# Optimization experiments

Measured on AMD Instinct MI355X. Metric: run time of the kernel, lower is better.

## Reference

```python
import jax, jax.numpy as jnp
import numpy as np
import math

B, S, D, H = 2, 2048, 2048, 16
DH = D // H  # 128

def setup_inputs() -> dict:
    key = jax.random.key(0)
    ks = jax.random.split(key, 5)
    x = jax.random.normal(ks[0], (B, S, D), dtype=jnp.float32)
    # causal mask: 1 where attendable, 0 where masked (masked_fill at mask==0)
    mask = jnp.tril(jnp.ones((S, S), dtype=jnp.int32))[None, None, :, :]
    wq = jax.random.normal(ks[1], (D, D), dtype=jnp.float32) * (1.0 / math.sqrt(D))
    wk = jax.random.normal(ks[2], (D, D), dtype=jnp.float32) * (1.0 / math.sqrt(D))
    wv = jax.random.normal(ks[3], (D, D), dtype=jnp.float32) * (1.0 / math.sqrt(D))
    wo = jax.random.normal(ks[4], (D, D), dtype=jnp.float32) * (1.0 / math.sqrt(D))
    return {"x": x, "mask": mask, "wq": wq, "wk": wk, "wv": wv, "wo": wo}

def reference(x, mask, wq, wk, wv, wo):
    b, s, d = x.shape
    # nn.Linear(d,d,bias=False): y = x @ W.T
    q = (x @ wq.T).reshape(b, s, H, DH).transpose(0, 2, 1, 3)  # [b,h,s,dh]
    k = (x @ wk.T).reshape(b, s, H, DH).transpose(0, 2, 1, 3)
    v = (x @ wv.T).reshape(b, s, H, DH).transpose(0, 2, 1, 3)
    scores = jnp.einsum('bhqd,bhkd->bhqk', q, k) / math.sqrt(DH)
    scores = jnp.where(mask == 0, jnp.float32(-1e9), scores)
    attn_weights = jax.nn.softmax(scores, axis=-1)
    attn_out = jnp.einsum('bhqk,bhkd->bhqd', attn_weights, v)
    attn_out = attn_out.transpose(0, 2, 1, 3).reshape(b, s, d)
    output = attn_out @ wo.T
    return (output, attn_weights)
```

## Files before the change

kernel.cpp:

```cpp
#include <hip/hip_runtime.h>
#include <hip/hip_bf16.h>
#include <cstdint>
#include <cstddef>

#define BATCH 2
#define S_LEN 2048
#define D_DIM 2048
#define NH 16
#define DHEAD 128
#define NXE ((size_t)BATCH * S_LEN * D_DIM)
#define NWE ((size_t)D_DIM * D_DIM)

typedef __bf16 bf16;
typedef __attribute__((ext_vector_type(8))) __bf16 bf16x8;
typedef __attribute__((ext_vector_type(4))) __bf16 bf16x4;
typedef __attribute__((ext_vector_type(4))) float f32x4;

__device__ __forceinline__ void async16(const void* g, void* l) {
  __builtin_amdgcn_global_load_lds((__attribute__((address_space(1))) void*)g,
                                   (__attribute__((address_space(3))) void*)l,
                                   16, 0, 0);
}

__global__ __launch_bounds__(256) void cast_kernel(const float4* __restrict__ in,
                                                   bf16x4* __restrict__ out, int n4) {
  int i = blockIdx.x * 256 + threadIdx.x;
  if (i < n4) {
    float4 v = in[i];
    bf16x4 o;
    o[0] = (bf16)v.x; o[1] = (bf16)v.y; o[2] = (bf16)v.z; o[3] = (bf16)v.w;
    out[i] = o;
  }
}

__global__ __launch_bounds__(256) void gemm_qkv(const bf16* __restrict__ A,
                                                const bf16* __restrict__ Wf,
                                                bf16* __restrict__ C0) {
  __shared__ __align__(16) bf16 As[128 * 32];
  __shared__ __align__(16) bf16 Bs[128 * 32];
  const int tid = threadIdx.x;
  const int wave = tid >> 6, lane = tid & 63;
  const int quad = lane >> 4, l16 = lane & 15;
  const int wm = (wave >> 1) * 64, wn = (wave & 1) * 64;
  const int m0 = blockIdx.y * 128, n0 = blockIdx.x * 128;
  const int K = D_DIM;

  f32x4 acc[4][4];
#pragma unroll
  for (int i = 0; i < 4; ++i)
#pragma unroll
    for (int j = 0; j < 4; ++j) acc[i][j] = (f32x4){0.f, 0.f, 0.f, 0.f};

  for (int k0 = 0; k0 < K; k0 += 32) {
    __syncthreads();
#pragma unroll
    for (int i = 0; i < 2; ++i) {
      int c = i * 256 + tid;
      int row = c & 127, k8 = c >> 7;
      async16(A + (size_t)(m0 + row) * K + k0 + k8 * 8, (void*)(As + (i * 256 + wave * 64) * 8));
      async16(Wf + (size_t)(n0 + row) * K + k0 + k8 * 8, (void*)(Bs + (i * 256 + wave * 64) * 8));
    }
    __builtin_amdgcn_s_waitcnt(0);
    __syncthreads();
    bf16x8 af[4], bfr[4];
#pragma unroll
    for (int i = 0; i < 4; ++i)
      af[i] = *(const bf16x8*)(As + (quad * 128 + wm + i * 16 + l16) * 8);
#pragma unroll
    for (int j = 0; j < 4; ++j)
      bfr[j] = *(const bf16x8*)(Bs + (quad * 128 + wn + j * 16 + l16) * 8);
#pragma unroll
    for (int i = 0; i < 4; ++i)
#pragma unroll
      for (int j = 0; j < 4; ++j)
        acc[i][j] = __builtin_amdgcn_mfma_f32_16x16x32_bf16(af[i], bfr[j], acc[i][j], 0, 0, 0);
  }
  const int mat = n0 >> 11;
  const int cb = n0 & 2047;
  bf16* Cm = C0 + (size_t)mat * NXE;
#pragma unroll
  for (int i = 0; i < 4; ++i)
#pragma unroll
    for (int j = 0; j < 4; ++j)
#pragma unroll
      for (int r = 0; r < 4; ++r) {
        int row = m0 + wm + i * 16 + quad * 4 + r;
        int col = cb + wn + j * 16 + l16;
        Cm[(size_t)row * D_DIM + col] = (bf16)acc[i][j][r];
      }
}

__global__ __launch_bounds__(256) void gemm_out(const bf16* __restrict__ A,
                                                const bf16* __restrict__ Bm,
                                                float* __restrict__ Cf) {
  __shared__ __align__(16) bf16 As[128 * 32];
  __shared__ __align__(16) bf16 Bs[128 * 32];
  const int tid = threadIdx.x;
  const int wave = tid >> 6, lane = tid & 63;
  const int quad = lane >> 4, l16 = lane & 15;
  const int wm = (wave >> 1) * 64, wn = (wave & 1) * 64;
  const int m0 = blockIdx.y * 128, n0 = blockIdx.x * 128;
  const int K = D_DIM, N = D_DIM;

  f32x4 acc[4][4];
#pragma unroll
  for (int i = 0; i < 4; ++i)
#pragma unroll
    for (int j = 0; j < 4; ++j) acc[i][j] = (f32x4){0.f, 0.f, 0.f, 0.f};

  for (int k0 = 0; k0 < K; k0 += 32) {
    __syncthreads();
#pragma unroll
    for (int i = 0; i < 2; ++i) {
      int c = i * 256 + tid;
      int row = c & 127, k8 = c >> 7;
      async16(A + (size_t)(m0 + row) * K + k0 + k8 * 8, (void*)(As + (i * 256 + wave * 64) * 8));
      async16(Bm + (size_t)(n0 + row) * K + k0 + k8 * 8, (void*)(Bs + (i * 256 + wave * 64) * 8));
    }
    __builtin_amdgcn_s_waitcnt(0);
    __syncthreads();
    bf16x8 af[4], bfr[4];
#pragma unroll
    for (int i = 0; i < 4; ++i)
      af[i] = *(const bf16x8*)(As + (quad * 128 + wm + i * 16 + l16) * 8);
#pragma unroll
    for (int j = 0; j < 4; ++j)
      bfr[j] = *(const bf16x8*)(Bs + (quad * 128 + wn + j * 16 + l16) * 8);
#pragma unroll
    for (int i = 0; i < 4; ++i)
#pragma unroll
      for (int j = 0; j < 4; ++j)
        acc[i][j] = __builtin_amdgcn_mfma_f32_16x16x32_bf16(af[i], bfr[j], acc[i][j], 0, 0, 0);
  }
#pragma unroll
  for (int i = 0; i < 4; ++i)
#pragma unroll
    for (int j = 0; j < 4; ++j)
#pragma unroll
      for (int r = 0; r < 4; ++r) {
        int row = m0 + wm + i * 16 + quad * 4 + r;
        int col = n0 + wn + j * 16 + l16;
        Cf[(size_t)row * N + col] = acc[i][j][r];
      }
}

__global__ __launch_bounds__(256) void transpose_v(const bf16* __restrict__ V,
                                                   bf16* __restrict__ Vt) {
  __shared__ __align__(16) bf16 tileT[64 * 80];
  const int tid = threadIdx.x;
  const int bh = blockIdx.z, b = bh >> 4, h = bh & 15;
  const int s0 = blockIdx.x * 64, d0 = blockIdx.y * 64;
  const int i = tid >> 3;
  const int jc = (tid & 7) * 8;
#pragma unroll
  for (int ii = 0; ii < 2; ++ii) {
    int si = i + ii * 32;
    bf16x8 v = *(const bf16x8*)(V + (size_t)(b * S_LEN + s0 + si) * D_DIM + h * DHEAD + d0 + jc);
#pragma unroll
    for (int u = 0; u < 8; ++u) tileT[(jc + u) * 80 + si] = v[u];
  }
  __syncthreads();
#pragma unroll
  for (int jj = 0; jj < 2; ++jj) {
    int jr = i + jj * 32;
    bf16x8 o = *(const bf16x8*)(tileT + jr * 80 + jc);
    *(bf16x8*)(Vt + ((size_t)bh * DHEAD + d0 + jr) * S_LEN + s0 + jc) = o;
  }
}

__global__ __launch_bounds__(256, 3) void attn_kernel(const bf16* __restrict__ Q,
                                                      const bf16* __restrict__ Kg,
                                                      const bf16* __restrict__ Vt,
                                                      float* __restrict__ P,
                                                      bf16* __restrict__ AO) {
  __shared__ __align__(16) bf16 KVs[128 * 128];
  __shared__ __align__(16) bf16 Ps[4][16 * 128];
  const int tid = threadIdx.x, wave = tid >> 6, lane = tid & 63;
  const int quad = lane >> 4, l16 = lane & 15;
  const int bh = blockIdx.y, b = bh >> 4, h = bh & 15;
  const int mt = (int)gridDim.x - 1 - (int)blockIdx.x;
  const int m0 = mt * 64;
  const int ntc = mt / 2 + 1;
  const bf16* Qh = Q + (size_t)b * S_LEN * D_DIM + h * DHEAD;
  const bf16* Kh = Kg + (size_t)b * S_LEN * D_DIM + h * DHEAD;
  const bf16* Vth = Vt + (size_t)bh * DHEAD * S_LEN;
  float* Pb = P + ((size_t)bh * S_LEN + m0) * S_LEN;
  const float scale = 0.08838834764831845f;

  bf16x8 aq[4];
  const bf16* qrow = Qh + (size_t)(m0 + wave * 16 + l16) * D_DIM + quad * 8;
#pragma unroll
  for (int kt = 0; kt < 4; ++kt) aq[kt] = *(const bf16x8*)(qrow + kt * 32);

  const int row_base = m0 + wave * 16 + quad * 4;
  float mrun[4], lrun[4];
#pragma unroll
  for (int r = 0; r < 4; ++r) { mrun[r] = -1e30f; lrun[r] = 0.f; }

  for (int t = 0; t < ntc; ++t) {
    const int n0 = t * 128;
    __syncthreads();
#pragma unroll
    for (int i = 0; i < 8; ++i) {
      int c = i * 256 + tid;
      int row = c & 127, k8 = c >> 7;
      async16(Kh + (size_t)(n0 + row) * D_DIM + k8 * 8, (void*)(KVs + (i * 256 + wave * 64) * 8));
    }
    __builtin_amdgcn_s_waitcnt(0);
    __syncthreads();
    f32x4 sacc[8];
#pragma unroll
    for (int jt = 0; jt < 8; ++jt) sacc[jt] = (f32x4){0.f, 0.f, 0.f, 0.f};
#pragma unroll
    for (int jt = 0; jt < 8; ++jt)
#pragma unroll
      for (int kt = 0; kt < 4; ++kt) {
        bf16x8 bk = *(const bf16x8*)(KVs + ((kt * 4 + quad) * 128 + jt * 16 + l16) * 8);
        sacc[jt] = __builtin_amdgcn_mfma_f32_16x16x32_bf16(aq[kt], bk, sacc[jt], 0, 0, 0);
      }
    const bool full = (n0 + 127 <= m0);
#pragma unroll
    for (int r = 0; r < 4; ++r) {
      const int rowg = row_base + r;
      float s[8], tmax = -3.0e38f;
#pragma unroll
      for (int jt = 0; jt < 8; ++jt) {
        float v = sacc[jt][r] * scale;
        if (!full) { int colg = n0 + jt * 16 + l16; v = (colg <= rowg) ? v : -3.0e38f; }
        s[jt] = v;
        tmax = fmaxf(tmax, v);
      }
      float mnew = fmaxf(mrun[r], tmax);
      float ps = 0.f;
#pragma unroll
      for (int jt = 0; jt < 8; ++jt) ps += __expf(s[jt] - mnew);
      lrun[r] = lrun[r] * __expf(mrun[r] - mnew) + ps;
      mrun[r] = mnew;
    }
  }
  float linv[4];
#pragma unroll
  for (int r = 0; r < 4; ++r) {
    float m = mrun[r], l = lrun[r];
#pragma unroll
    for (int off = 1; off < 16; off <<= 1) {
      float mo = __shfl_xor(m, off);
      float lo = __shfl_xor(l, off);
      float mn = fmaxf(m, mo);
      l = l * __expf(m - mn) + lo * __expf(mo - mn);
      m = mn;
    }
    mrun[r] = m;
    linv[r] = 1.0f / l;
  }

  f32x4 oacc[8];
#pragma unroll
  for (int jt = 0; jt < 8; ++jt) oacc[jt] = (f32x4){0.f, 0.f, 0.f, 0.f};
  bf16* myPs = Ps[wave];

  for (int t = 0; t < 16; ++t) {
    const int n0 = t * 128;
    if (t < ntc) {
      __syncthreads();
#pragma unroll
      for (int i = 0; i < 8; ++i) {
        int c = i * 256 + tid;
        int row = c & 127, k8 = c >> 7;
        async16(Kh + (size_t)(n0 + row) * D_DIM + k8 * 8, (void*)(KVs + (i * 256 + wave * 64) * 8));
      }
      __builtin_amdgcn_s_waitcnt(0);
      __syncthreads();
      f32x4 sacc[8];
#pragma unroll
      for (int jt = 0; jt < 8; ++jt) sacc[jt] = (f32x4){0.f, 0.f, 0.f, 0.f};
#pragma unroll
      for (int jt = 0; jt < 8; ++jt)
#pragma unroll
        for (int kt = 0; kt < 4; ++kt) {
          bf16x8 bk = *(const bf16x8*)(KVs + ((kt * 4 + quad) * 128 + jt * 16 + l16) * 8);
          sacc[jt] = __builtin_amdgcn_mfma_f32_16x16x32_bf16(aq[kt], bk, sacc[jt], 0, 0, 0);
        }
      const bool full = (n0 + 127 <= m0);
#pragma unroll
      for (int jt = 0; jt < 8; ++jt)
#pragma unroll
        for (int r = 0; r < 4; ++r) {
          float e = __expf(sacc[jt][r] * scale - mrun[r]) * linv[r];
          if (!full) {
            int colg = n0 + jt * 16 + l16;
            e = (colg <= row_base + r) ? e : 0.f;
          }
          int kk = jt * 16 + l16, m = quad * 4 + r;
          myPs[((kk >> 3) * 16 + m) * 8 + (kk & 7)] = (bf16)e;
        }
      asm volatile("s_waitcnt lgkmcnt(0)" ::: "memory");
      bf16x8 ap[4];
#pragma unroll
      for (int kt = 0; kt < 4; ++kt)
        ap[kt] = *(const bf16x8*)(myPs + ((kt * 4 + quad) * 16 + l16) * 8);
#pragma unroll
      for (int i = 0; i < 8; ++i) {
        int idx = i * 64 + lane;
        int row = idx >> 5, c0 = (idx & 31) * 4;
        bf16x4 pv = *(const bf16x4*)(myPs + ((c0 >> 3) * 16 + row) * 8 + (c0 & 7));
        float4 o = make_float4((float)pv[0], (float)pv[1], (float)pv[2], (float)pv[3]);
        *(float4*)(Pb + (size_t)(wave * 16 + row) * S_LEN + n0 + c0) = o;
      }
      __syncthreads();
#pragma unroll
      for (int i = 0; i < 8; ++i) {
        int c = i * 256 + tid;
        int row = c & 127, k8 = c >> 7;
        async16(Vth + (size_t)row * S_LEN + n0 + k8 * 8, (void*)(KVs + (i * 256 + wave * 64) * 8));
      }
      __builtin_amdgcn_s_waitcnt(0);
      __syncthreads();
#pragma unroll
      for (int jt = 0; jt < 8; ++jt)
#pragma unroll
        for (int kt = 0; kt < 4; ++kt) {
          bf16x8 bv = *(const bf16x8*)(KVs + ((kt * 4 + quad) * 128 + jt * 16 + l16) * 8);
          oacc[jt] = __builtin_amdgcn_mfma_f32_16x16x32_bf16(ap[kt], bv, oacc[jt], 0, 0, 0);
        }
    } else {
      float4 z = make_float4(0.f, 0.f, 0.f, 0.f);
#pragma unroll
      for (int i = 0; i < 8; ++i) {
        int idx = i * 256 + tid;
        int row = idx >> 5, c4 = idx & 31;
        *(float4*)(Pb + (size_t)row * S_LEN + n0 + c4 * 4) = z;
      }
    }
  }
  bf16* AOb = AO + ((size_t)(b * S_LEN + m0 + wave * 16 + quad * 4)) * D_DIM + h * DHEAD;
#pragma unroll
  for (int jt = 0; jt < 8; ++jt)
#pragma unroll
    for (int r = 0; r < 4; ++r)
      AOb[(size_t)r * D_DIM + jt * 16 + l16] = (bf16)oacc[jt][r];
}

extern "C" void kernel_launch(void* const* d_in, const int* in_sizes, int n_in,
                              void* d_out, int out_size, void* d_ws, size_t ws_size,
                              hipStream_t stream) {
  const float* x  = (const float*)d_in[0];
  const float* wq = (const float*)d_in[2];
  const float* wk = (const float*)d_in[3];
  const float* wv = (const float*)d_in[4];
  const float* wo = (const float*)d_in[5];
  float* out = (float*)d_out;

  bf16* ws = (bf16*)d_ws;
  bf16* Xb = ws;
  bf16* Wq = Xb + NXE;
  bf16* Wk = Wq + NWE;
  bf16* Wv = Wk + NWE;
  bf16* Wo = Wv + NWE;
  bf16* Qm = Wo + NWE;
  bf16* Km = Qm + NXE;
  bf16* Vm = Km + NXE;
  bf16* Vt = Vm + NXE;
  bf16* AOm = Vt + NXE;

  cast_kernel<<<(int)(NXE / 4 / 256), 256, 0, stream>>>((const float4*)x, (bf16x4*)Xb, (int)(NXE / 4));
  cast_kernel<<<(int)(NWE / 4 / 256), 256, 0, stream>>>((const float4*)wq, (bf16x4*)Wq, (int)(NWE / 4));
  cast_kernel<<<(int)(NWE / 4 / 256), 256, 0, stream>>>((const float4*)wk, (bf16x4*)Wk, (int)(NWE / 4));
  cast_kernel<<<(int)(NWE / 4 / 256), 256, 0, stream>>>((const float4*)wv, (bf16x4*)Wv, (int)(NWE / 4));
  cast_kernel<<<(int)(NWE / 4 / 256), 256, 0, stream>>>((const float4*)wo, (bf16x4*)Wo, (int)(NWE / 4));

  gemm_qkv<<<dim3(3 * D_DIM / 128, BATCH * S_LEN / 128), 256, 0, stream>>>(Xb, Wq, Qm);

  transpose_v<<<dim3(S_LEN / 64, DHEAD / 64, BATCH * NH), 256, 0, stream>>>(Vm, Vt);

  attn_kernel<<<dim3(S_LEN / 64, BATCH * NH), 256, 0, stream>>>(Qm, Km, Vt, out + NXE, AOm);

  gemm_out<<<dim3(D_DIM / 128, BATCH * S_LEN / 128), 256, 0, stream>>>(AOm, Wo, out);
}
```

Baseline: 1.231 ms.

## Load K/V tiles directly from global memory and remap grid for XCD locality

Removes the shared-memory staging of K and V tiles in the attention kernel, along with the block-wide barriers around it. Each wave now loads its MFMA B operands straight from global memory and relies on the L2 cache for reuse across the four waves. The grid becomes 1D, with block ids remapped so that all query tiles of a given head land on the same XCD, which should improve L2 hit rates. The cost is redundant global loads per wave and less latency hiding, in exchange for fewer barriers, less LDS use and possibly higher occupancy.

```diff
diff --git a/kernel.cpp b/kernel.cpp
--- a/kernel.cpp
+++ b/kernel.cpp
@@ -173,12 +173,14 @@
                                                       const bf16* __restrict__ Vt,
                                                       float* __restrict__ P,
                                                       bf16* __restrict__ AO) {
-  __shared__ __align__(16) bf16 KVs[128 * 128];
   __shared__ __align__(16) bf16 Ps[4][16 * 128];
   const int tid = threadIdx.x, wave = tid >> 6, lane = tid & 63;
   const int quad = lane >> 4, l16 = lane & 15;
-  const int bh = blockIdx.y, b = bh >> 4, h = bh & 15;
-  const int mt = (int)gridDim.x - 1 - (int)blockIdx.x;
+  const int bid = blockIdx.x;
+  const int xcd = bid & 7, sidx = bid >> 3;
+  const int bh = xcd * 4 + (sidx >> 5);
+  const int mt = 31 - (sidx & 31);
+  const int b = bh >> 4, h = bh & 15;
   const int m0 = mt * 64;
   const int ntc = mt / 2 + 1;
   const bf16* Qh = Q + (size_t)b * S_LEN * D_DIM + h * DHEAD;
@@ -199,25 +201,18 @@
 
   for (int t = 0; t < ntc; ++t) {
     const int n0 = t * 128;
-    __syncthreads();
-#pragma unroll
-    for (int i = 0; i < 8; ++i) {
-      int c = i * 256 + tid;
-      int row = c & 127, k8 = c >> 7;
-      async16(Kh + (size_t)(n0 + row) * D_DIM + k8 * 8, (void*)(KVs + (i * 256 + wave * 64) * 8));
-    }
-    __builtin_amdgcn_s_waitcnt(0);
-    __syncthreads();
     f32x4 sacc[8];
 #pragma unroll
     for (int jt = 0; jt < 8; ++jt) sacc[jt] = (f32x4){0.f, 0.f, 0.f, 0.f};
 #pragma unroll
-    for (int jt = 0; jt < 8; ++jt)
+    for (int jt = 0; jt < 8; ++jt) {
+      const bf16* kb = Kh + (size_t)(n0 + jt * 16 + l16) * D_DIM + quad * 8;
 #pragma unroll
       for (int kt = 0; kt < 4; ++kt) {
-        bf16x8 bk = *(const bf16x8*)(KVs + ((kt * 4 + quad) * 128 + jt * 16 + l16) * 8);
+        bf16x8 bk = *(const bf16x8*)(kb + kt * 32);
         sacc[jt] = __builtin_amdgcn_mfma_f32_16x16x32_bf16(aq[kt], bk, sacc[jt], 0, 0, 0);
       }
+    }
     const bool full = (n0 + 127 <= m0);
 #pragma unroll
     for (int r = 0; r < 4; ++r) {
@@ -262,25 +257,18 @@
   for (int t = 0; t < 16; ++t) {
     const int n0 = t * 128;
     if (t < ntc) {
-      __syncthreads();
-#pragma unroll
-      for (int i = 0; i < 8; ++i) {
-        int c = i * 256 + tid;
-        int row = c & 127, k8 = c >> 7;
-        async16(Kh + (size_t)(n0 + row) * D_DIM + k8 * 8, (void*)(KVs + (i * 256 + wave * 64) * 8));
-      }
-      __builtin_amdgcn_s_waitcnt(0);
-      __syncthreads();
       f32x4 sacc[8];
 #pragma unroll
       for (int jt = 0; jt < 8; ++jt) sacc[jt] = (f32x4){0.f, 0.f, 0.f, 0.f};
 #pragma unroll
-      for (int jt = 0; jt < 8; ++jt)
+      for (int jt = 0; jt < 8; ++jt) {
+        const bf16* kb = Kh + (size_t)(n0 + jt * 16 + l16) * D_DIM + quad * 8;
 #pragma unroll
         for (int kt = 0; kt < 4; ++kt) {
-          bf16x8 bk = *(const bf16x8*)(KVs + ((kt * 4 + quad) * 128 + jt * 16 + l16) * 8);
+          bf16x8 bk = *(const bf16x8*)(kb + kt * 32);
           sacc[jt] = __builtin_amdgcn_mfma_f32_16x16x32_bf16(aq[kt], bk, sacc[jt], 0, 0, 0);
         }
+      }
       const bool full = (n0 + 127 <= m0);
 #pragma unroll
       for (int jt = 0; jt < 8; ++jt)
@@ -299,6 +287,7 @@
 #pragma unroll
       for (int kt = 0; kt < 4; ++kt)
         ap[kt] = *(const bf16x8*)(myPs + ((kt * 4 + quad) * 16 + l16) * 8);
+      asm volatile("s_waitcnt lgkmcnt(0)" ::: "memory");
 #pragma unroll
       for (int i = 0; i < 8; ++i) {
         int idx = i * 64 + lane;
@@ -307,22 +296,15 @@
         float4 o = make_float4((float)pv[0], (float)pv[1], (float)pv[2], (float)pv[3]);
         *(float4*)(Pb + (size_t)(wave * 16 + row) * S_LEN + n0 + c0) = o;
       }
-      __syncthreads();
-#pragma unroll
-      for (int i = 0; i < 8; ++i) {
-        int c = i * 256 + tid;
-        int row = c & 127, k8 = c >> 7;
-        async16(Vth + (size_t)row * S_LEN + n0 + k8 * 8, (void*)(KVs + (i * 256 + wave * 64) * 8));
-      }
-      __builtin_amdgcn_s_waitcnt(0);
-      __syncthreads();
-#pragma unroll
-      for (int jt = 0; jt < 8; ++jt)
+#pragma unroll
+      for (int jt = 0; jt < 8; ++jt) {
+        const bf16* vb = Vth + (size_t)(jt * 16 + l16) * S_LEN + n0 + quad * 8;
 #pragma unroll
         for (int kt = 0; kt < 4; ++kt) {
-          bf16x8 bv = *(const bf16x8*)(KVs + ((kt * 4 + quad) * 128 + jt * 16 + l16) * 8);
+          bf16x8 bv = *(const bf16x8*)(vb + kt * 32);
           oacc[jt] = __builtin_amdgcn_mfma_f32_16x16x32_bf16(ap[kt], bv, oacc[jt], 0, 0, 0);
         }
+      }
     } else {
       float4 z = make_float4(0.f, 0.f, 0.f, 0.f);
 #pragma unroll
@@ -373,7 +355,7 @@
 
   transpose_v<<<dim3(S_LEN / 64, DHEAD / 64, BATCH * NH), 256, 0, stream>>>(Vm, Vt);
 
-  attn_kernel<<<dim3(S_LEN / 64, BATCH * NH), 256, 0, stream>>>(Qm, Km, Vt, out + NXE, AOm);
+  attn_kernel<<<dim3(1024), 256, 0, stream>>>(Qm, Km, Vt, out + NXE, AOm);
 
   gemm_out<<<dim3(D_DIM / 128, BATCH * S_LEN / 128), 256, 0, stream>>>(AOm, Wo, out);
 }
```

New measurement: 1.424 ms. 15.7% more time.
